# Performance work log

Hardware: AMD Instinct MI355X
Metric: run time of the kernel (lower is better)

The kernel has to match this reference:

```python
import jax, jax.numpy as jnp
import numpy as np

WINDOW_SIZE = 11
SIGMA = 1.5
C1 = 0.01 ** 2
C2 = 0.03 ** 2


def _gaussian_1d(window_size, sigma):
    x = np.arange(window_size, dtype=np.float32)
    g = np.exp(-((x - window_size // 2) ** 2) / (2.0 * sigma ** 2))
    g = g / g.sum()
    return jnp.asarray(g, dtype=jnp.float32)


def _blur(x, g1d):
    # Separable depthwise Gaussian blur, SAME padding.
    # x: [B, C, H, W]; mathematically identical to conv with outer(g, g).
    c = x.shape[1]
    pad = WINDOW_SIZE // 2
    kh = jnp.broadcast_to(g1d.reshape(1, 1, WINDOW_SIZE, 1), (c, 1, WINDOW_SIZE, 1))
    kw = jnp.broadcast_to(g1d.reshape(1, 1, 1, WINDOW_SIZE), (c, 1, 1, WINDOW_SIZE))
    dn = ('NCHW', 'OIHW', 'NCHW')
    x = jax.lax.conv_general_dilated(x, kh, (1, 1), [(pad, pad), (0, 0)],
                                     dimension_numbers=dn, feature_group_count=c)
    x = jax.lax.conv_general_dilated(x, kw, (1, 1), [(0, 0), (pad, pad)],
                                     dimension_numbers=dn, feature_group_count=c)
    return x


def setup_inputs() -> dict:
    key = jax.random.key(0)
    k1, k2 = jax.random.split(key)
    shape = (32, 1, 512, 512)
    img1 = jax.random.uniform(k1, shape, dtype=jnp.float32)
    img2 = jax.random.uniform(k2, shape, dtype=jnp.float32)
    return {"img1": img1, "img2": img2}


def reference(img1, img2):
    g1d = _gaussian_1d(WINDOW_SIZE, SIGMA)
    mu1 = _blur(img1, g1d)
    mu2 = _blur(img2, g1d)
    mu1_sq = mu1 * mu1
    mu2_sq = mu2 * mu2
    mu1_mu2 = mu1 * mu2
    sigma1_sq = _blur(img1 * img1, g1d) - mu1_sq
    sigma2_sq = _blur(img2 * img2, g1d) - mu2_sq
    sigma12 = _blur(img1 * img2, g1d) - mu1_mu2
    ssim_map = ((2.0 * mu1_mu2 + C1) * (2.0 * sigma12 + C2)) / (
        (mu1_sq + mu2_sq + C1) * (sigma1_sq + sigma2_sq + C2))
    return ssim_map.mean()  # size_average=True
```

## Files before the change

### kernel.cpp

```cpp
#include <hip/hip_runtime.h>

#define HH 512
#define WW 512
#define BATCH 32
#define BH 16
#define NB (HH / BH)
#define TPB 256
#define NBLOCKS (NB * BATCH)
#define PW 528
#define CBASE 0xAAAAAAAAu


typedef float f2 __attribute__((ext_vector_type(2)));

__global__ __launch_bounds__(TPB) void ssim_main(
    const float* __restrict__ img1,
    const float* __restrict__ img2,
    unsigned* __restrict__ counter,
    float* __restrict__ partial,
    float* __restrict__ out)
{
  constexpr float G[11] = {
      0.00102838f, 0.00759876f, 0.03600077f, 0.10936070f, 0.21300553f,
      0.26601171f,
      0.21300553f, 0.10936070f, 0.03600077f, 0.00759876f, 0.00102838f};
  constexpr float C1 = 1.0e-4f;
  constexpr float C2 = 9.0e-4f;

  const int tid  = threadIdx.x;
  const int band = blockIdx.x;
  const int bat  = blockIdx.y;
  const int r0   = band * BH;
  const float* p1 = img1 + (size_t)bat * (HH * WW);
  const float* p2 = img2 + (size_t)bat * (HH * WW);
  const int c0 = tid * 2;

  __shared__ __align__(16) float sp[5 * PW * 2];

  if (tid < 80) {
    const int a = tid >> 4, s = tid & 15;
    const int idx = (s < 9) ? s : (512 + s);
    *(f2*)(sp + a * (2 * PW) + 2 * idx) = f2{0.f, 0.f};
  }

  float2 w1[12], w2[12];
#pragma unroll
  for (int j = 0; j < 12; ++j) {
    const int r = r0 - 5 + j;
    float2 a = make_float2(0.f, 0.f), b = a;
    if (r >= 0 && r < HH) {
      a = *(const float2*)(p1 + r * WW + c0);
      b = *(const float2*)(p2 + r * WW + c0);
    }
    w1[j] = a; w2[j] = b;
  }

  __syncthreads();

  float ssum = 0.f;

#pragma unroll 1
  for (int q = 0; q < BH; q += 2) {
    float2 ta1 = make_float2(0.f, 0.f), ta2 = ta1, tb1 = ta1, tb2 = ta1;
    if (q + 2 < BH) {
      const int ra = r0 + 7 + q;
      const int rb = r0 + 8 + q;
      if (ra < HH) {
        ta1 = *(const float2*)(p1 + ra * WW + c0);
        ta2 = *(const float2*)(p2 + ra * WW + c0);
      }
      if (rb < HH) {
        tb1 = *(const float2*)(p1 + rb * WW + c0);
        tb2 = *(const float2*)(p2 + rb * WW + c0);
      }
    }

    f2 acc2[5][2];
#pragma unroll
    for (int a = 0; a < 5; ++a) { acc2[a][0] = f2{0.f, 0.f}; acc2[a][1] = f2{0.f, 0.f}; }

#pragma unroll
    for (int e = 0; e < 12; ++e) {
      const f2 g2 = f2{(e < 11) ? G[e] : 0.f, (e > 0) ? G[e - 1] : 0.f};
      const float xv[2] = {w1[e].x, w1[e].y};
      const float yv[2] = {w2[e].x, w2[e].y};
#pragma unroll
      for (int i = 0; i < 2; ++i) {
        const float x = xv[i], y = yv[i];
        const float xx = x * x, yy = y * y, xy = x * y;
        acc2[0][i] = __builtin_elementwise_fma(g2, f2{x,  x},  acc2[0][i]);
        acc2[1][i] = __builtin_elementwise_fma(g2, f2{y,  y},  acc2[1][i]);
        acc2[2][i] = __builtin_elementwise_fma(g2, f2{xx, xx}, acc2[2][i]);
        acc2[3][i] = __builtin_elementwise_fma(g2, f2{yy, yy}, acc2[3][i]);
        acc2[4][i] = __builtin_elementwise_fma(g2, f2{xy, xy}, acc2[4][i]);
      }
    }

#pragma unroll
    for (int a = 0; a < 5; ++a) {
      float* base = sp + a * (2 * PW) + 4 * tid + 18;
      *(f2*)(base)     = acc2[a][0];
      *(f2*)(base + 2) = acc2[a][1];
    }

    __syncthreads();

    f2 h2[5][2];
#pragma unroll
    for (int a = 0; a < 5; ++a) {
      const float* base = sp + a * (2 * PW);
      f2 t2[12];
#pragma unroll
      for (int m = 0; m < 6; ++m) {
        const float4 X = *(const float4*)(base + 4 * tid + 8 + 4 * m);
        t2[2 * m]     = f2{X.x, X.y};
        t2[2 * m + 1] = f2{X.z, X.w};
      }
#pragma unroll
      for (int j = 0; j < 2; ++j) {
        f2 hv = f2{0.f, 0.f};
#pragma unroll
        for (int k = 0; k < 11; ++k)
          hv = __builtin_elementwise_fma(f2{G[k], G[k]}, t2[j + k], hv);
        h2[a][j] = hv;
      }
    }

#pragma unroll
    for (int j = 0; j < 2; ++j) {
      const f2 mu1 = h2[0][j], mu2 = h2[1][j];
      const f2 mu12 = mu1 * mu2;
      const f2 den1 = __builtin_elementwise_fma(
          mu1, mu1, __builtin_elementwise_fma(mu2, mu2, f2{C1, C1}));
      const f2 vs   = (h2[2][j] + h2[3][j]) - den1 + f2{C1 + C2, C1 + C2};
      const f2 sg12 = h2[4][j] - mu12;
      const f2 num = (mu12 + mu12 + f2{C1, C1}) * (sg12 + sg12 + f2{C2, C2});
      const f2 den = den1 * vs;
      float rn0 = __builtin_amdgcn_rcpf(den.x);
      float rn1 = __builtin_amdgcn_rcpf(den.y);
      rn0 = rn0 * fmaf(-den.x, rn0, 2.0f);
      rn1 = rn1 * fmaf(-den.y, rn1, 2.0f);
      ssum = fmaf(num.x, rn0, ssum);
      ssum = fmaf(num.y, rn1, ssum);
    }

    __syncthreads();

#pragma unroll
    for (int j = 0; j < 10; ++j) { w1[j] = w1[j + 2]; w2[j] = w2[j + 2]; }
    w1[10] = ta1; w2[10] = ta2;
    w1[11] = tb1; w2[11] = tb2;
  }

#pragma unroll
  for (int off = 32; off > 0; off >>= 1) ssum += __shfl_xor(ssum, off, 64);
  float*  wred = sp;
  double* dred = (double*)(sp + 8);
  int*    flag = (int*)(sp + 16);
  const int wid = tid >> 6;
  if ((tid & 63) == 0) wred[wid] = ssum;
  __syncthreads();
  if (tid == 0) {
    const float bsum = wred[0] + wred[1] + wred[2] + wred[3];
    atomicExch(&partial[bat * NB + band], bsum);
    __threadfence();
    const unsigned old = atomicAdd(counter, 1u);
    flag[0] = (old == CBASE + (unsigned)NBLOCKS - 1u) ? 1 : 0;
  }
  __syncthreads();
  if (flag[0]) {
    double s = 0.0;
    for (int i = tid; i < NBLOCKS; i += TPB)
      s += (double)atomicAdd(&partial[i], 0.0f);
#pragma unroll
    for (int off = 32; off > 0; off >>= 1) s += __shfl_xor(s, off, 64);
    if ((tid & 63) == 0) dred[wid] = s;
    __syncthreads();
    if (tid == 0)
      out[0] = (float)((dred[0] + dred[1] + dred[2] + dred[3]) /
                       (double)((size_t)BATCH * HH * WW));
  }
}

extern "C" void kernel_launch(void* const* d_in, const int* in_sizes, int n_in,
                              void* d_out, int out_size, void* d_ws, size_t ws_size,
                              hipStream_t stream) {
  const float* img1 = (const float*)d_in[0];
  const float* img2 = (const float*)d_in[1];
  float* out = (float*)d_out;
  unsigned* counter = (unsigned*)d_ws;
  float* partial = (float*)((char*)d_ws + 16);
  dim3 grid(NB, BATCH);
  ssim_main<<<grid, TPB, 0, stream>>>(img1, img2, counter, partial, out);
}
```

Before: 127.7 us.

## Software-pipeline vertical blur of next row pair ahead of horizontal pass

Computes the vertical Gaussian accumulators for the next pair of rows in registers while the current pair's horizontal blur and SSIM math run, then stores them to shared memory after the barrier. The row window grows to 14 rows and the prefetch distance moves ahead by two rows. This aims to overlap ALU work with LDS latency, at the cost of extra registers that may lower occupancy or cause spills.

Result: slower. 131.1 us (+2.7%).

```diff
diff --git a/kernel.cpp b/kernel.cpp
--- a/kernel.cpp
+++ b/kernel.cpp
@@ -12,6 +12,41 @@
 
 
 typedef float f2 __attribute__((ext_vector_type(2)));
+
+#define VERT(ACC, O)                                                          \
+  do {                                                                        \
+    _Pragma("unroll")                                                         \
+    for (int a = 0; a < 5; ++a) {                                             \
+      ACC[a][0] = f2{0.f, 0.f};                                               \
+      ACC[a][1] = f2{0.f, 0.f};                                               \
+    }                                                                         \
+    _Pragma("unroll")                                                         \
+    for (int e = 0; e < 12; ++e) {                                            \
+      const f2 g2 = f2{(e < 11) ? G[e] : 0.f, (e > 0) ? G[e - 1] : 0.f};      \
+      const float xv[2] = {w1[(O) + e].x, w1[(O) + e].y};                     \
+      const float yv[2] = {w2[(O) + e].x, w2[(O) + e].y};                     \
+      _Pragma("unroll")                                                       \
+      for (int i = 0; i < 2; ++i) {                                           \
+        const float x = xv[i], y = yv[i];                                     \
+        const float xx = x * x, yy = y * y, xy = x * y;                       \
+        ACC[0][i] = __builtin_elementwise_fma(g2, f2{x, x}, ACC[0][i]);       \
+        ACC[1][i] = __builtin_elementwise_fma(g2, f2{y, y}, ACC[1][i]);       \
+        ACC[2][i] = __builtin_elementwise_fma(g2, f2{xx, xx}, ACC[2][i]);     \
+        ACC[3][i] = __builtin_elementwise_fma(g2, f2{yy, yy}, ACC[3][i]);     \
+        ACC[4][i] = __builtin_elementwise_fma(g2, f2{xy, xy}, ACC[4][i]);     \
+      }                                                                       \
+    }                                                                         \
+  } while (0)
+
+#define STORE_ACC(ACC)                                                        \
+  do {                                                                        \
+    _Pragma("unroll")                                                         \
+    for (int a = 0; a < 5; ++a) {                                             \
+      float* base = sp + a * (2 * PW) + 4 * tid + 18;        \
+      *(f2*)(base) = ACC[a][0];                                               \
+      *(f2*)(base + 2) = ACC[a][1];                                           \
+    }                                                                         \
+  } while (0)
 
 __global__ __launch_bounds__(TPB) void ssim_main(
     const float* __restrict__ img1,
@@ -43,9 +78,9 @@
     *(f2*)(sp + a * (2 * PW) + 2 * idx) = f2{0.f, 0.f};
   }
 
-  float2 w1[12], w2[12];
-#pragma unroll
-  for (int j = 0; j < 12; ++j) {
+  float2 w1[14], w2[14];
+#pragma unroll
+  for (int j = 0; j < 14; ++j) {
     const int r = r0 - 5 + j;
     float2 a = make_float2(0.f, 0.f), b = a;
     if (r >= 0 && r < HH) {
@@ -55,16 +90,22 @@
     w1[j] = a; w2[j] = b;
   }
 
-  __syncthreads();
+  {
+    f2 accC[5][2];
+    VERT(accC, 0);
+    STORE_ACC(accC);
+  }
 
   float ssum = 0.f;
 
 #pragma unroll 1
   for (int q = 0; q < BH; q += 2) {
+    __syncthreads();
+
     float2 ta1 = make_float2(0.f, 0.f), ta2 = ta1, tb1 = ta1, tb2 = ta1;
-    if (q + 2 < BH) {
-      const int ra = r0 + 7 + q;
-      const int rb = r0 + 8 + q;
+    if (q + 4 < BH) {
+      const int ra = r0 + q + 9;
+      const int rb = r0 + q + 10;
       if (ra < HH) {
         ta1 = *(const float2*)(p1 + ra * WW + c0);
         ta2 = *(const float2*)(p2 + ra * WW + c0);
@@ -74,36 +115,6 @@
         tb2 = *(const float2*)(p2 + rb * WW + c0);
       }
     }
-
-    f2 acc2[5][2];
-#pragma unroll
-    for (int a = 0; a < 5; ++a) { acc2[a][0] = f2{0.f, 0.f}; acc2[a][1] = f2{0.f, 0.f}; }
-
-#pragma unroll
-    for (int e = 0; e < 12; ++e) {
-      const f2 g2 = f2{(e < 11) ? G[e] : 0.f, (e > 0) ? G[e - 1] : 0.f};
-      const float xv[2] = {w1[e].x, w1[e].y};
-      const float yv[2] = {w2[e].x, w2[e].y};
-#pragma unroll
-      for (int i = 0; i < 2; ++i) {
-        const float x = xv[i], y = yv[i];
-        const float xx = x * x, yy = y * y, xy = x * y;
-        acc2[0][i] = __builtin_elementwise_fma(g2, f2{x,  x},  acc2[0][i]);
-        acc2[1][i] = __builtin_elementwise_fma(g2, f2{y,  y},  acc2[1][i]);
-        acc2[2][i] = __builtin_elementwise_fma(g2, f2{xx, xx}, acc2[2][i]);
-        acc2[3][i] = __builtin_elementwise_fma(g2, f2{yy, yy}, acc2[3][i]);
-        acc2[4][i] = __builtin_elementwise_fma(g2, f2{xy, xy}, acc2[4][i]);
-      }
-    }
-
-#pragma unroll
-    for (int a = 0; a < 5; ++a) {
-      float* base = sp + a * (2 * PW) + 4 * tid + 18;
-      *(f2*)(base)     = acc2[a][0];
-      *(f2*)(base + 2) = acc2[a][1];
-    }
-
-    __syncthreads();
 
     f2 h2[5][2];
 #pragma unroll
@@ -124,6 +135,11 @@
           hv = __builtin_elementwise_fma(f2{G[k], G[k]}, t2[j + k], hv);
         h2[a][j] = hv;
       }
+    }
+
+    f2 accN[5][2];
+    if (q + 2 < BH) {
+      VERT(accN, 2);
     }
 
 #pragma unroll
@@ -146,10 +162,14 @@
 
     __syncthreads();
 
-#pragma unroll
-    for (int j = 0; j < 10; ++j) { w1[j] = w1[j + 2]; w2[j] = w2[j + 2]; }
-    w1[10] = ta1; w2[10] = ta2;
-    w1[11] = tb1; w2[11] = tb2;
+    if (q + 2 < BH) {
+      STORE_ACC(accN);
+    }
+
+#pragma unroll
+    for (int j = 0; j < 12; ++j) { w1[j] = w1[j + 2]; w2[j] = w2[j + 2]; }
+    w1[12] = ta1; w2[12] = ta2;
+    w1[13] = tb1; w2[13] = tb2;
   }
 
 #pragma unroll
```

## Do horizontal blur from global loads and vertical blur in a register ring

Applied to the files above, without the earlier changes.

The kernel swaps its order: the horizontal 11-tap pass now runs first, on a 16-wide window each thread loads directly from global memory. The vertical pass runs over an 11-row ring buffer of horizontal results kept in registers, so the shared-memory staging and per-iteration barriers go away. The whole 26-row loop is fully unrolled. In exchange each row is loaded about 8 times across neighbouring threads (relying on cache), register pressure rises sharply, and the modulo ring indexing only stays in registers if the compiler resolves it at compile time.

After: 242.2 us. +89.7%, slower.

```diff
diff --git a/kernel.cpp b/kernel.cpp
--- a/kernel.cpp
+++ b/kernel.cpp
@@ -7,7 +7,6 @@
 #define NB (HH / BH)
 #define TPB 256
 #define NBLOCKS (NB * BATCH)
-#define PW 528
 #define CBASE 0xAAAAAAAAu
 
 
@@ -34,106 +33,76 @@
   const float* p1 = img1 + (size_t)bat * (HH * WW);
   const float* p2 = img2 + (size_t)bat * (HH * WW);
   const int c0 = tid * 2;
+  const int s0 = c0 - 6;
+  const bool fast = (c0 >= 6) && (c0 <= 502);
 
-  __shared__ __align__(16) float sp[5 * PW * 2];
-
-  if (tid < 80) {
-    const int a = tid >> 4, s = tid & 15;
-    const int idx = (s < 9) ? s : (512 + s);
-    *(f2*)(sp + a * (2 * PW) + 2 * idx) = f2{0.f, 0.f};
-  }
-
-  float2 w1[12], w2[12];
-#pragma unroll
-  for (int j = 0; j < 12; ++j) {
-    const int r = r0 - 5 + j;
-    float2 a = make_float2(0.f, 0.f), b = a;
-    if (r >= 0 && r < HH) {
-      a = *(const float2*)(p1 + r * WW + c0);
-      b = *(const float2*)(p2 + r * WW + c0);
-    }
-    w1[j] = a; w2[j] = b;
-  }
-
-  __syncthreads();
+  f2 hw[11][5];
 
   float ssum = 0.f;
 
-#pragma unroll 1
-  for (int q = 0; q < BH; q += 2) {
-    float2 ta1 = make_float2(0.f, 0.f), ta2 = ta1, tb1 = ta1, tb2 = ta1;
-    if (q + 2 < BH) {
-      const int ra = r0 + 7 + q;
-      const int rb = r0 + 8 + q;
-      if (ra < HH) {
-        ta1 = *(const float2*)(p1 + ra * WW + c0);
-        ta2 = *(const float2*)(p2 + ra * WW + c0);
+#pragma unroll
+  for (int rr = 0; rr < BH + 10; ++rr) {
+    const int r = r0 - 5 + rr;
+    f2 ha = f2{0.f, 0.f}, hb = ha, hc = ha, hd = ha, he = ha;
+
+    if (r >= 0 && r < HH) {
+      float w1[16], w2[16];
+      if (fast) {
+        const float* a1 = p1 + r * WW + s0;
+        const float* a2 = p2 + r * WW + s0;
+#pragma unroll
+        for (int m = 0; m < 8; ++m) {
+          *(f2*)(w1 + 2 * m) = *(const f2*)(a1 + 2 * m);
+          *(f2*)(w2 + 2 * m) = *(const f2*)(a2 + 2 * m);
+        }
+      } else {
+#pragma unroll
+        for (int j = 0; j < 16; ++j) { w1[j] = 0.f; w2[j] = 0.f; }
+#pragma unroll
+        for (int j = 1; j <= 12; ++j) {
+          const int col = s0 + j;
+          if (col >= 0 && col < WW) {
+            w1[j] = p1[r * WW + col];
+            w2[j] = p2[r * WW + col];
+          }
+        }
       }
-      if (rb < HH) {
-        tb1 = *(const float2*)(p1 + rb * WW + c0);
-        tb2 = *(const float2*)(p2 + rb * WW + c0);
+#pragma unroll
+      for (int k = 0; k < 11; ++k) {
+        const f2 g2 = f2{G[k], G[k]};
+        const f2 x = f2{w1[k + 1], w1[k + 2]};
+        const f2 y = f2{w2[k + 1], w2[k + 2]};
+        ha = __builtin_elementwise_fma(g2, x, ha);
+        hb = __builtin_elementwise_fma(g2, y, hb);
+        hc = __builtin_elementwise_fma(g2, x * x, hc);
+        hd = __builtin_elementwise_fma(g2, y * y, hd);
+        he = __builtin_elementwise_fma(g2, x * y, he);
       }
     }
 
-    f2 acc2[5][2];
-#pragma unroll
-    for (int a = 0; a < 5; ++a) { acc2[a][0] = f2{0.f, 0.f}; acc2[a][1] = f2{0.f, 0.f}; }
-
-#pragma unroll
-    for (int e = 0; e < 12; ++e) {
-      const f2 g2 = f2{(e < 11) ? G[e] : 0.f, (e > 0) ? G[e - 1] : 0.f};
-      const float xv[2] = {w1[e].x, w1[e].y};
-      const float yv[2] = {w2[e].x, w2[e].y};
-#pragma unroll
-      for (int i = 0; i < 2; ++i) {
-        const float x = xv[i], y = yv[i];
-        const float xx = x * x, yy = y * y, xy = x * y;
-        acc2[0][i] = __builtin_elementwise_fma(g2, f2{x,  x},  acc2[0][i]);
-        acc2[1][i] = __builtin_elementwise_fma(g2, f2{y,  y},  acc2[1][i]);
-        acc2[2][i] = __builtin_elementwise_fma(g2, f2{xx, xx}, acc2[2][i]);
-        acc2[3][i] = __builtin_elementwise_fma(g2, f2{yy, yy}, acc2[3][i]);
-        acc2[4][i] = __builtin_elementwise_fma(g2, f2{xy, xy}, acc2[4][i]);
-      }
+    {
+      const int sl = rr % 11;
+      hw[sl][0] = ha; hw[sl][1] = hb; hw[sl][2] = hc;
+      hw[sl][3] = hd; hw[sl][4] = he;
     }
 
+    if (rr >= 10) {
+      f2 m1 = f2{0.f, 0.f}, m2 = m1, sxx = m1, syy = m1, sxy = m1;
 #pragma unroll
-    for (int a = 0; a < 5; ++a) {
-      float* base = sp + a * (2 * PW) + 4 * tid + 18;
-      *(f2*)(base)     = acc2[a][0];
-      *(f2*)(base + 2) = acc2[a][1];
-    }
-
-    __syncthreads();
-
-    f2 h2[5][2];
-#pragma unroll
-    for (int a = 0; a < 5; ++a) {
-      const float* base = sp + a * (2 * PW);
-      f2 t2[12];
-#pragma unroll
-      for (int m = 0; m < 6; ++m) {
-        const float4 X = *(const float4*)(base + 4 * tid + 8 + 4 * m);
-        t2[2 * m]     = f2{X.x, X.y};
-        t2[2 * m + 1] = f2{X.z, X.w};
+      for (int d = 0; d < 11; ++d) {
+        const int s = (rr - 10 + d) % 11;
+        const f2 g2 = f2{G[d], G[d]};
+        m1  = __builtin_elementwise_fma(g2, hw[s][0], m1);
+        m2  = __builtin_elementwise_fma(g2, hw[s][1], m2);
+        sxx = __builtin_elementwise_fma(g2, hw[s][2], sxx);
+        syy = __builtin_elementwise_fma(g2, hw[s][3], syy);
+        sxy = __builtin_elementwise_fma(g2, hw[s][4], sxy);
       }
-#pragma unroll
-      for (int j = 0; j < 2; ++j) {
-        f2 hv = f2{0.f, 0.f};
-#pragma unroll
-        for (int k = 0; k < 11; ++k)
-          hv = __builtin_elementwise_fma(f2{G[k], G[k]}, t2[j + k], hv);
-        h2[a][j] = hv;
-      }
-    }
-
-#pragma unroll
-    for (int j = 0; j < 2; ++j) {
-      const f2 mu1 = h2[0][j], mu2 = h2[1][j];
-      const f2 mu12 = mu1 * mu2;
+      const f2 mu12 = m1 * m2;
       const f2 den1 = __builtin_elementwise_fma(
-          mu1, mu1, __builtin_elementwise_fma(mu2, mu2, f2{C1, C1}));
-      const f2 vs   = (h2[2][j] + h2[3][j]) - den1 + f2{C1 + C2, C1 + C2};
-      const f2 sg12 = h2[4][j] - mu12;
+          m1, m1, __builtin_elementwise_fma(m2, m2, f2{C1, C1}));
+      const f2 vs   = (sxx + syy) - den1 + f2{C1 + C2, C1 + C2};
+      const f2 sg12 = sxy - mu12;
       const f2 num = (mu12 + mu12 + f2{C1, C1}) * (sg12 + sg12 + f2{C2, C2});
       const f2 den = den1 * vs;
       float rn0 = __builtin_amdgcn_rcpf(den.x);
@@ -143,20 +112,13 @@
       ssum = fmaf(num.x, rn0, ssum);
       ssum = fmaf(num.y, rn1, ssum);
     }
-
-    __syncthreads();
-
-#pragma unroll
-    for (int j = 0; j < 10; ++j) { w1[j] = w1[j + 2]; w2[j] = w2[j + 2]; }
-    w1[10] = ta1; w2[10] = ta2;
-    w1[11] = tb1; w2[11] = tb2;
   }
 
+  __shared__ float  wred[4];
+  __shared__ double dred[4];
+  __shared__ int    flag;
 #pragma unroll
   for (int off = 32; off > 0; off >>= 1) ssum += __shfl_xor(ssum, off, 64);
-  float*  wred = sp;
-  double* dred = (double*)(sp + 8);
-  int*    flag = (int*)(sp + 16);
   const int wid = tid >> 6;
   if ((tid & 63) == 0) wred[wid] = ssum;
   __syncthreads();
@@ -165,10 +127,10 @@
     atomicExch(&partial[bat * NB + band], bsum);
     __threadfence();
     const unsigned old = atomicAdd(counter, 1u);
-    flag[0] = (old == CBASE + (unsigned)NBLOCKS - 1u) ? 1 : 0;
+    flag = (old == CBASE + (unsigned)NBLOCKS - 1u) ? 1 : 0;
   }
   __syncthreads();
-  if (flag[0]) {
+  if (flag) {
     double s = 0.0;
     for (int i = tid; i < NBLOCKS; i += TPB)
       s += (double)atomicAdd(&partial[i], 0.0f);
```
